# Optimization experiments

Hardware: AMD Instinct MI355X
Metric: run time of the kernel (lower is better)

Reference implementation:

```python
import jax, jax.numpy as jnp
import numpy as np

NU = 60000   # num_users
NI = 40000   # num_items
N = NU + NI  # num_nodes
E = 2000000  # num_edges
F = 128      # feat_dim (user_feat_dim == item_feat_dim)
H = 128      # hidden_dim


def setup_inputs() -> dict:
    key = jax.random.key(0)
    ks = jax.random.split(key, 14)
    s = 0.05
    inp = {
        "x": jax.random.normal(ks[0], (N, F), jnp.float32),
        "edge_index": jax.random.randint(ks[1], (2, E), 0, N, dtype=jnp.int32),
        "node_type": jnp.concatenate([jnp.zeros(NU, jnp.int32), jnp.ones(NI, jnp.int32)]),
        # input projections (Linear stores weight as (out, in))
        "w_user": s * jax.random.normal(ks[2], (H, F), jnp.float32),
        "b_user": jnp.zeros((H,), jnp.float32),
        "w_item": s * jax.random.normal(ks[3], (H, F), jnp.float32),
        "b_item": jnp.zeros((H,), jnp.float32),
        # SAGEConv layer 0: lin_l (aggregated neighbors, with bias), lin_r (root, no bias)
        "w_l0": s * jax.random.normal(ks[4], (H, H), jnp.float32),
        "b_l0": s * jax.random.normal(ks[5], (H,), jnp.float32),
        "w_r0": s * jax.random.normal(ks[6], (H, H), jnp.float32),
        # SAGEConv layer 1
        "w_l1": s * jax.random.normal(ks[7], (H, H), jnp.float32),
        "b_l1": s * jax.random.normal(ks[8], (H,), jnp.float32),
        "w_r1": s * jax.random.normal(ks[9], (H, H), jnp.float32),
    }
    return inp


def _sage_conv(h, src, dst, w_l, b_l, w_r):
    # gather source features, max-aggregate onto destinations (PyG aggr='max')
    msg = h[src]                                          # [E, H]
    agg = jax.ops.segment_max(msg, dst, num_segments=N)   # [N, H], -inf where no in-edges
    agg = jnp.where(jnp.isneginf(agg), 0.0, agg)          # PyG fills empty segments with 0
    return agg @ w_l.T + b_l + h @ w_r.T


def reference(x, edge_index, node_type, w_user, b_user, w_item, b_item,
              w_l0, b_l0, w_r0, w_l1, b_l1, w_r1):
    # node_type is sorted: first NU rows are users, rest are items
    src, dst = edge_index[0], edge_index[1]
    user_h = x[:NU] @ w_user.T + b_user                   # [NU, H]
    item_h = x[NU:] @ w_item.T + b_item                   # [NI, H]
    h = jnp.concatenate([user_h, item_h], axis=0)         # [N, H]
    # layer 0 with residual (dims match) then ReLU; dropout is identity in eval
    h = h + _sage_conv(h, src, dst, w_l0, b_l0, w_r0)
    h = jax.nn.relu(h)
    # layer 1 with residual (no activation after last layer)
    h = h + _sage_conv(h, src, dst, w_l1, b_l1, w_r1)
    return (h[:NU], h[NU:])
```

## Files before the change

kernel.cpp:

```cpp
#include <hip/hip_runtime.h>

#define NUSR 60000
#define NITM 40000
#define NN   100000
#define EE   2000000
#define HD   128

#define BW   512
#define NB   196
#define EPB  8192

using bf16x8   = __attribute__((ext_vector_type(8))) short;
using f32x4    = __attribute__((ext_vector_type(4))) float;
using ushort4t = __attribute__((ext_vector_type(4))) unsigned short;
using ushort2t = __attribute__((ext_vector_type(2))) unsigned short;
using ushort8t = __attribute__((ext_vector_type(8))) unsigned short;
using uint4t   = __attribute__((ext_vector_type(4))) unsigned int;

__device__ __forceinline__ unsigned short f2bf(float f) {
    unsigned int u = __float_as_uint(f);
    u += 0x7FFFu + ((u >> 16) & 1u);
    return (unsigned short)(u >> 16);
}
__device__ __forceinline__ float bf2f(unsigned short s) {
    return __uint_as_float(((unsigned int)s) << 16);
}
__device__ __forceinline__ unsigned short keyof(unsigned short b) {
    return (b & 0x8000u) ? (unsigned short)~b : (unsigned short)(b | 0x8000u);
}
__device__ __forceinline__ unsigned unkey32(unsigned k) {
    unsigned negsel = (~k & 0x80008000u) >> 15;
    return k ^ (0x80008000u | (negsel * 0x7FFFu));
}
__device__ __forceinline__ int swz(int row, int col) {
    return row * HD + (col ^ ((row & 7) << 3));
}
__device__ __forceinline__ ushort8t pkmax8(ushort8t a, ushort8t b) {
    return __builtin_elementwise_max(a, b);
}

__global__ __launch_bounds__(256) void bhist_k(const int* __restrict__ dst,
                                               int* __restrict__ bcnt) {
    __shared__ int h[NB];
    int t = threadIdx.x;
    if (t < NB) h[t] = 0;
    __syncthreads();
    int e0 = blockIdx.x * EPB;
    #pragma unroll 4
    for (int i = t; i < EPB; i += 256) {
        int e = e0 + i;
        if (e < EE) atomicAdd(&h[dst[e] >> 9], 1);
    }
    __syncthreads();
    if (t < NB && h[t]) atomicAdd(&bcnt[t], h[t]);
}

__global__ void bscan_k(const int* __restrict__ bcnt, int* __restrict__ bbase,
                        int* __restrict__ bcur, int* __restrict__ off) {
    __shared__ int s[256];
    int t = threadIdx.x;
    int v = (t < NB) ? bcnt[t] : 0;
    s[t] = v;
    __syncthreads();
    for (int d = 1; d < 256; d <<= 1) {
        int a = (t >= d) ? s[t - d] : 0;
        __syncthreads();
        s[t] += a;
        __syncthreads();
    }
    if (t < NB) { bbase[t] = s[t] - v; bcur[t] = s[t] - v; }
    if (t == NB - 1) { bbase[NB] = s[t]; off[NN] = EE; }
}

__global__ __launch_bounds__(256) void bscatter_k(const int* __restrict__ src,
                                                  const int* __restrict__ dst,
                                                  int* __restrict__ bcur,
                                                  unsigned int* __restrict__ bedge) {
    __shared__ int h[NB], base[NB];
    int t = threadIdx.x;
    if (t < NB) h[t] = 0;
    __syncthreads();
    int e0 = blockIdx.x * EPB;
    #pragma unroll 4
    for (int i = t; i < EPB; i += 256) {
        int e = e0 + i;
        if (e < EE) atomicAdd(&h[dst[e] >> 9], 1);
    }
    __syncthreads();
    if (t < NB) {
        int c = h[t];
        base[t] = c ? atomicAdd(&bcur[t], c) : 0;
        h[t] = 0;
    }
    __syncthreads();
    #pragma unroll 4
    for (int i = t; i < EPB; i += 256) {
        int e = e0 + i;
        if (e < EE) {
            int d = dst[e];
            int b = d >> 9;
            int p = base[b] + atomicAdd(&h[b], 1);
            bedge[p] = ((unsigned)(d - (b << 9)) << 17) | (unsigned)src[e];
        }
    }
}

__global__ __launch_bounds__(512) void bcsr_k(const unsigned int* __restrict__ bedge,
                                              const int* __restrict__ bbase,
                                              int* __restrict__ off,
                                              int* __restrict__ csr) {
    __shared__ int cnt[BW], cur[BW], sc[BW];
    int b = blockIdx.x, t = threadIdx.x;
    int n0 = b * BW;
    int nloc = min(BW, NN - n0);
    cnt[t] = 0;
    __syncthreads();
    int e0 = bbase[b], e1 = bbase[b + 1];
    for (int e = e0 + t; e < e1; e += 512)
        atomicAdd(&cnt[bedge[e] >> 17], 1);
    __syncthreads();
    int v = cnt[t];
    sc[t] = v;
    __syncthreads();
    for (int d = 1; d < BW; d <<= 1) {
        int a = (t >= d) ? sc[t - d] : 0;
        __syncthreads();
        sc[t] += a;
        __syncthreads();
    }
    int excl = sc[t] - v;
    if (t < nloc) { off[n0 + t] = e0 + excl; cur[t] = e0 + excl; }
    __syncthreads();
    for (int e = e0 + t; e < e1; e += 512) {
        unsigned ed = bedge[e];
        int p = atomicAdd(&cur[ed >> 17], 1);
        csr[p] = (int)(ed & 0x1FFFFu);
    }
}

__global__ void cvt6_k(const float* __restrict__ a0, const float* __restrict__ a1,
                       const float* __restrict__ a2, const float* __restrict__ a3,
                       const float* __restrict__ a4, const float* __restrict__ a5,
                       unsigned short* __restrict__ out) {
    int i = blockIdx.x * 256 + threadIdx.x;
    const float* s;
    switch (i >> 14) {
        case 0: s = a0; break; case 1: s = a1; break; case 2: s = a2; break;
        case 3: s = a3; break; case 4: s = a4; break; default: s = a5; break;
    }
    out[i] = f2bf(s[i & 16383]);
}

__global__ __launch_bounds__(256) void proj_mfma_k(
    const float* __restrict__ x, const unsigned short* __restrict__ wb,
    const float* __restrict__ bias, unsigned short* __restrict__ hkey,
    int row_base, int nrows) {
    __shared__ unsigned short lw[HD * HD];
    int tid = threadIdx.x;
    #pragma unroll
    for (int it = 0; it < 16; ++it) {
        int flat = (it * 256 + tid) * 4;
        int row = flat >> 7, col = flat & 127;
        *(ushort4t*)&lw[swz(row, col)] = *(const ushort4t*)(wb + flat);
    }
    __syncthreads();
    int lane = tid & 63, w = tid >> 6;
    int l15 = lane & 15, l4 = lane >> 4;
    int m0 = blockIdx.x * 128 + w * 32;
    f32x4 acc[2][8] = {};
    #pragma unroll
    for (int kb = 0; kb < 4; ++kb) {
        bf16x8 a[2];
        #pragma unroll
        for (int rt = 0; rt < 2; ++rt) {
            int r = m0 + rt * 16 + l15;
            if (r >= nrows) r = nrows - 1;
            const float* ap = x + (size_t)(row_base + r) * HD + kb * 32 + l4 * 8;
            f32x4 v0 = *(const f32x4*)ap;
            f32x4 v1 = *(const f32x4*)(ap + 4);
            bf16x8 f;
            #pragma unroll
            for (int j = 0; j < 4; ++j) { f[j] = (short)f2bf(v0[j]); f[j + 4] = (short)f2bf(v1[j]); }
            a[rt] = f;
        }
        #pragma unroll
        for (int ct = 0; ct < 8; ++ct) {
            bf16x8 b = *(const bf16x8*)&lw[swz(ct * 16 + l15, kb * 32 + l4 * 8)];
            acc[0][ct] = __builtin_amdgcn_mfma_f32_16x16x32_bf16(a[0], b, acc[0][ct], 0, 0, 0);
            acc[1][ct] = __builtin_amdgcn_mfma_f32_16x16x32_bf16(a[1], b, acc[1][ct], 0, 0, 0);
        }
    }
    __syncthreads();
    #pragma unroll
    for (int ct = 0; ct < 8; ++ct) {
        int col = ct * 16 + l15;
        float bv = bias[col];
        #pragma unroll
        for (int rt = 0; rt < 2; ++rt)
            #pragma unroll
            for (int j = 0; j < 4; ++j) {
                int lrow = w * 32 + rt * 16 + l4 * 4 + j;
                lw[lrow * HD + ((col + ((lrow & 15) << 3)) & 127)] =
                    keyof(f2bf(acc[rt][ct][j] + bv));
            }
    }
    __syncthreads();
    int row = tid >> 1, cb = (tid & 1) * 64;
    int r = blockIdx.x * 128 + row;
    if (r < nrows) {
        int sof = (row & 15) << 3;
        #pragma unroll
        for (int gg = 0; gg < 8; ++gg) {
            uint4t v = *(const uint4t*)&lw[row * HD + ((cb + gg * 8 + sof) & 127)];
            *(uint4t*)(hkey + (size_t)(row_base + r) * HD + cb + gg * 8) = v;
        }
    }
}

__global__ __launch_bounds__(256) void agg_key_k(
    const uint4t* __restrict__ hkey4,
    const int* __restrict__ off, const int* __restrict__ csr,
    uint4t* __restrict__ agg4) {
    int node = (blockIdx.x * 256 + threadIdx.x) >> 6;
    int lane = threadIdx.x & 63;
    if (node >= NN) return;
    int s0 = off[node], s1 = off[node + 1];
    int deg = s1 - s0;
    int q = lane >> 4, l16 = lane & 15;
    ushort8t m = {0, 0, 0, 0, 0, 0, 0, 0};
    int cval = (lane < deg) ? csr[s0 + lane] : 0;
    int nslots = deg < 64 ? deg : 64;
    #pragma unroll
    for (int u = 0; u < 16; ++u) {
        int idx = u * 4 + q;
        int r = __shfl(cval, idx, 64);
        if (idx < nslots) {
            uint4t v = hkey4[(size_t)r * 16 + l16];
            m = pkmax8(m, *(ushort8t*)&v);
        }
    }
    for (int base = s0 + 64; base < s1; base += 32) {
        #pragma unroll
        for (int u = 0; u < 8; ++u) {
            int jj = base + u * 4 + q;
            if (jj < s1) {
                int r = csr[jj];
                uint4t v = hkey4[(size_t)r * 16 + l16];
                m = pkmax8(m, *(ushort8t*)&v);
            }
        }
    }
    uint4t mu = *(uint4t*)&m;
    #pragma unroll
    for (int c = 0; c < 4; ++c) {
        unsigned a = mu[c];
        unsigned b = (unsigned)__shfl_xor((int)a, 16, 64);
        ushort2t pa = *(ushort2t*)&a, pb = *(ushort2t*)&b;
        pa = __builtin_elementwise_max(pa, pb);
        a = *(unsigned*)&pa;
        b = (unsigned)__shfl_xor((int)a, 32, 64);
        pb = *(ushort2t*)&b;
        pa = __builtin_elementwise_max(pa, pb);
        mu[c] = *(unsigned*)&pa;
    }
    if (q == 0) {
        uint4t outv = {0, 0, 0, 0};
        if (deg > 0) {
            #pragma unroll
            for (int c = 0; c < 4; ++c) outv[c] = unkey32(mu[c]);
        }
        agg4[(size_t)node * 16 + l16] = outv;
    }
}

__global__ __launch_bounds__(256) void combine_mfma_k(
    const unsigned short* __restrict__ hkey, const unsigned short* __restrict__ aggb,
    const unsigned short* __restrict__ wlb, const float* __restrict__ bl,
    const unsigned short* __restrict__ wrb,
    unsigned short* __restrict__ hkey_out, float* __restrict__ fout, int relu) {
    __shared__ unsigned short lw[2][HD * HD];
    int tid = threadIdx.x;
    #pragma unroll
    for (int it = 0; it < 16; ++it) {
        int flat = (it * 256 + tid) * 4;
        int row = flat >> 7, col = flat & 127;
        *(ushort4t*)&lw[0][swz(row, col)] = *(const ushort4t*)(wlb + flat);
        *(ushort4t*)&lw[1][swz(row, col)] = *(const ushort4t*)(wrb + flat);
    }
    __syncthreads();
    int lane = tid & 63, w = tid >> 6;
    int l15 = lane & 15, l4 = lane >> 4;
    int m0 = blockIdx.x * 128 + w * 32;
    const uint4t* hk4 = (const uint4t*)hkey;
    f32x4 acc[2][8] = {};
    #pragma unroll
    for (int kb = 0; kb < 4; ++kb) {
        bf16x8 a1[2], a2[2];
        #pragma unroll
        for (int rt = 0; rt < 2; ++rt) {
            int r = m0 + rt * 16 + l15;
            if (r >= NN) r = NN - 1;
            size_t o = (size_t)r * HD + kb * 32 + l4 * 8;
            a1[rt] = *(const bf16x8*)(aggb + o);
            uint4t aw = hk4[(size_t)r * 16 + kb * 4 + l4];
            bf16x8 f;
            #pragma unroll
            for (int u = 0; u < 4; ++u) {
                unsigned d = unkey32(aw[u]);
                f[2 * u]     = (short)(d & 0xFFFFu);
                f[2 * u + 1] = (short)(d >> 16);
            }
            a2[rt] = f;
        }
        #pragma unroll
        for (int ct = 0; ct < 8; ++ct) {
            bf16x8 b1 = *(const bf16x8*)&lw[0][swz(ct * 16 + l15, kb * 32 + l4 * 8)];
            bf16x8 b2 = *(const bf16x8*)&lw[1][swz(ct * 16 + l15, kb * 32 + l4 * 8)];
            acc[0][ct] = __builtin_amdgcn_mfma_f32_16x16x32_bf16(a1[0], b1, acc[0][ct], 0, 0, 0);
            acc[0][ct] = __builtin_amdgcn_mfma_f32_16x16x32_bf16(a2[0], b2, acc[0][ct], 0, 0, 0);
            acc[1][ct] = __builtin_amdgcn_mfma_f32_16x16x32_bf16(a1[1], b1, acc[1][ct], 0, 0, 0);
            acc[1][ct] = __builtin_amdgcn_mfma_f32_16x16x32_bf16(a2[1], b2, acc[1][ct], 0, 0, 0);
        }
    }
    __syncthreads();
    float* cs = (float*)lw;
    #pragma unroll
    for (int ct = 0; ct < 8; ++ct)
        #pragma unroll
        for (int rt = 0; rt < 2; ++rt)
            #pragma unroll
            for (int j = 0; j < 4; ++j) {
                int lrow = w * 32 + rt * 16 + l4 * 4 + j;
                int col = ct * 16 + l15;
                cs[lrow * HD + ((col + lrow) & 127)] = acc[rt][ct][j];
            }
    __syncthreads();
    int row = tid >> 1, cb = (tid & 1) * 64;
    int r = blockIdx.x * 128 + row;
    if (r < NN) {
        const uint4t* resrow = (const uint4t*)(hkey + (size_t)r * HD + cb);
        uint4t res[8];
        #pragma unroll
        for (int g = 0; g < 8; ++g) res[g] = resrow[g];
        if (fout) {
            #pragma unroll
            for (int gg = 0; gg < 8; ++gg) {
                f32x4 va, vb;
                #pragma unroll
                for (int u = 0; u < 4; ++u) {
                    int c0 = cb + gg * 8 + u * 2;
                    unsigned d = unkey32(res[gg][u]);
                    float v0 = cs[row * HD + ((c0 + row) & 127)] + bl[c0]
                             + bf2f((unsigned short)(d & 0xFFFFu));
                    float v1 = cs[row * HD + ((c0 + 1 + row) & 127)] + bl[c0 + 1]
                             + bf2f((unsigned short)(d >> 16));
                    if (relu) { v0 = fmaxf(v0, 0.0f); v1 = fmaxf(v1, 0.0f); }
                    if (u < 2) { va[u * 2] = v0; va[u * 2 + 1] = v1; }
                    else       { vb[(u - 2) * 2] = v0; vb[(u - 2) * 2 + 1] = v1; }
                }
                *(f32x4*)(fout + (size_t)r * HD + cb + gg * 8) = va;
                *(f32x4*)(fout + (size_t)r * HD + cb + gg * 8 + 4) = vb;
            }
        } else {
            #pragma unroll
            for (int gg = 0; gg < 8; ++gg) {
                uint4t ov;
                #pragma unroll
                for (int u = 0; u < 4; ++u) {
                    int c0 = cb + gg * 8 + u * 2;
                    unsigned d = unkey32(res[gg][u]);
                    float v0 = cs[row * HD + ((c0 + row) & 127)] + bl[c0]
                             + bf2f((unsigned short)(d & 0xFFFFu));
                    float v1 = cs[row * HD + ((c0 + 1 + row) & 127)] + bl[c0 + 1]
                             + bf2f((unsigned short)(d >> 16));
                    if (relu) { v0 = fmaxf(v0, 0.0f); v1 = fmaxf(v1, 0.0f); }
                    ov[u] = (unsigned)keyof(f2bf(v0)) | ((unsigned)keyof(f2bf(v1)) << 16);
                }
                *(uint4t*)(hkey_out + (size_t)r * HD + cb + gg * 8) = ov;
            }
        }
    }
}

extern "C" void kernel_launch(void* const* d_in, const int* in_sizes, int n_in,
                              void* d_out, int out_size, void* d_ws, size_t ws_size,
                              hipStream_t stream) {
    const float* x      = (const float*)d_in[0];
    const int*   ei     = (const int*)d_in[1];
    const float* w_user = (const float*)d_in[3];
    const float* b_user = (const float*)d_in[4];
    const float* w_item = (const float*)d_in[5];
    const float* b_item = (const float*)d_in[6];
    const float* w_l0   = (const float*)d_in[7];
    const float* b_l0   = (const float*)d_in[8];
    const float* w_r0   = (const float*)d_in[9];
    const float* w_l1   = (const float*)d_in[10];
    const float* b_l1   = (const float*)d_in[11];
    const float* w_r1   = (const float*)d_in[12];

    const int* e_src = ei;
    const int* e_dst = ei + EE;

    char* ws = (char*)d_ws;
    size_t cur_off = 0;
    auto carve = [&](size_t bytes) {
        void* p = ws + cur_off;
        cur_off = (cur_off + bytes + 255) & ~(size_t)255;
        return p;
    };
    unsigned short* hkey0 = (unsigned short*)carve((size_t)NN * HD * 2);
    unsigned short* hkey1 = (unsigned short*)carve((size_t)NN * HD * 2);
    unsigned short* aggb  = (unsigned short*)carve((size_t)NN * HD * 2);
    unsigned short* wb    = (unsigned short*)carve((size_t)6 * HD * HD * 2);
    int*      off   = (int*)carve((size_t)(NN + 1) * 4);
    int*      csr   = (int*)carve((size_t)EE * 4);
    unsigned* bedge = (unsigned*)carve((size_t)EE * 4);
    int*      bcnt  = (int*)carve((NB + 1) * 4);
    int*      bbase = (int*)carve((NB + 1) * 4);
    int*      bcur  = (int*)carve((NB + 1) * 4);
    (void)ws_size;

    hipMemsetAsync(bcnt, 0, (size_t)NB * 4, stream);
    int nbB = (EE + EPB - 1) / EPB;
    bhist_k<<<nbB, 256, 0, stream>>>(e_dst, bcnt);
    bscan_k<<<1, 256, 0, stream>>>(bcnt, bbase, bcur, off);
    bscatter_k<<<nbB, 256, 0, stream>>>(e_src, e_dst, bcur, bedge);
    bcsr_k<<<NB, 512, 0, stream>>>(bedge, bbase, off, csr);

    cvt6_k<<<(6 * HD * HD) / 256, 256, 0, stream>>>(w_user, w_item, w_l0, w_r0, w_l1, w_r1, wb);

    proj_mfma_k<<<(NUSR + 127) / 128, 256, 0, stream>>>(x, wb,         b_user, hkey0, 0,    NUSR);
    proj_mfma_k<<<(NITM + 127) / 128, 256, 0, stream>>>(x, wb + 16384, b_item, hkey0, NUSR, NITM);

    agg_key_k<<<NN / 4, 256, 0, stream>>>((const uint4t*)hkey0, off, csr, (uint4t*)aggb);
    combine_mfma_k<<<(NN + 127) / 128, 256, 0, stream>>>(
        hkey0, aggb, wb + 2 * 16384, b_l0, wb + 3 * 16384, hkey1, nullptr, 1);

    agg_key_k<<<NN / 4, 256, 0, stream>>>((const uint4t*)hkey1, off, csr, (uint4t*)aggb);
    combine_mfma_k<<<(NN + 127) / 128, 256, 0, stream>>>(
        hkey1, aggb, wb + 4 * 16384, b_l1, wb + 5 * 16384, nullptr, (float*)d_out, 0);
}
```

Before: 313.2 us.

## Double combine block to 256 rows and vectorize epilogue with two-phase LDS staging

```diff
diff --git a/kernel.cpp b/kernel.cpp
--- a/kernel.cpp
+++ b/kernel.cpp
@@ -273,7 +273,7 @@
     }
 }
 
-__global__ __launch_bounds__(256) void combine_mfma_k(
+__global__ __launch_bounds__(512) void combine_mfma_k(
     const unsigned short* __restrict__ hkey, const unsigned short* __restrict__ aggb,
     const unsigned short* __restrict__ wlb, const float* __restrict__ bl,
     const unsigned short* __restrict__ wrb,
@@ -281,8 +281,8 @@
     __shared__ unsigned short lw[2][HD * HD];
     int tid = threadIdx.x;
     #pragma unroll
-    for (int it = 0; it < 16; ++it) {
-        int flat = (it * 256 + tid) * 4;
+    for (int it = 0; it < 8; ++it) {
+        int flat = (it * 512 + tid) * 4;
         int row = flat >> 7, col = flat & 127;
         *(ushort4t*)&lw[0][swz(row, col)] = *(const ushort4t*)(wlb + flat);
         *(ushort4t*)&lw[1][swz(row, col)] = *(const ushort4t*)(wrb + flat);
@@ -290,7 +290,7 @@
     __syncthreads();
     int lane = tid & 63, w = tid >> 6;
     int l15 = lane & 15, l4 = lane >> 4;
-    int m0 = blockIdx.x * 128 + w * 32;
+    int m0 = blockIdx.x * 256 + w * 32;
     const uint4t* hk4 = (const uint4t*)hkey;
     f32x4 acc[2][8] = {};
     #pragma unroll
@@ -324,61 +324,64 @@
     }
     __syncthreads();
     float* cs = (float*)lw;
-    #pragma unroll
-    for (int ct = 0; ct < 8; ++ct)
-        #pragma unroll
-        for (int rt = 0; rt < 2; ++rt)
-            #pragma unroll
-            for (int j = 0; j < 4; ++j) {
-                int lrow = w * 32 + rt * 16 + l4 * 4 + j;
-                int col = ct * 16 + l15;
-                cs[lrow * HD + ((col + lrow) & 127)] = acc[rt][ct][j];
-            }
-    __syncthreads();
-    int row = tid >> 1, cb = (tid & 1) * 64;
-    int r = blockIdx.x * 128 + row;
-    if (r < NN) {
-        const uint4t* resrow = (const uint4t*)(hkey + (size_t)r * HD + cb);
-        uint4t res[8];
-        #pragma unroll
-        for (int g = 0; g < 8; ++g) res[g] = resrow[g];
-        if (fout) {
-            #pragma unroll
-            for (int gg = 0; gg < 8; ++gg) {
-                f32x4 va, vb;
+    for (int p = 0; p < 2; ++p) {
+        if ((w >> 2) == p) {
+            #pragma unroll
+            for (int ct = 0; ct < 8; ++ct)
+                #pragma unroll
+                for (int rt = 0; rt < 2; ++rt)
+                    #pragma unroll
+                    for (int j = 0; j < 4; ++j) {
+                        int lrow = (w & 3) * 32 + rt * 16 + l4 * 4 + j;
+                        int col = ct * 16 + l15;
+                        cs[lrow * HD + ((col + lrow * 4) & 127)] = acc[rt][ct][j];
+                    }
+        }
+        __syncthreads();
+        int lrow = tid >> 2, cq = (tid & 3) * 32;
+        int r = blockIdx.x * 256 + p * 128 + lrow;
+        if (r < NN) {
+            const float* crow = cs + lrow * HD;
+            int rot = lrow * 4;
+            #pragma unroll
+            for (int gg = 0; gg < 4; ++gg) {
+                int c0 = cq + gg * 8;
+                uint4t res = *(const uint4t*)(hkey + (size_t)r * HD + c0);
+                f32x4 cv0 = *(const f32x4*)&crow[(c0 + rot) & 127];
+                f32x4 cv1 = *(const f32x4*)&crow[(c0 + 4 + rot) & 127];
+                f32x4 bv0 = *(const f32x4*)(bl + c0);
+                f32x4 bv1 = *(const f32x4*)(bl + c0 + 4);
+                float v[8];
                 #pragma unroll
                 for (int u = 0; u < 4; ++u) {
-                    int c0 = cb + gg * 8 + u * 2;
-                    unsigned d = unkey32(res[gg][u]);
-                    float v0 = cs[row * HD + ((c0 + row) & 127)] + bl[c0]
-                             + bf2f((unsigned short)(d & 0xFFFFu));
-                    float v1 = cs[row * HD + ((c0 + 1 + row) & 127)] + bl[c0 + 1]
-                             + bf2f((unsigned short)(d >> 16));
-                    if (relu) { v0 = fmaxf(v0, 0.0f); v1 = fmaxf(v1, 0.0f); }
-                    if (u < 2) { va[u * 2] = v0; va[u * 2 + 1] = v1; }
-                    else       { vb[(u - 2) * 2] = v0; vb[(u - 2) * 2 + 1] = v1; }
+                    unsigned d = unkey32(res[u]);
+                    float c_lo = (u < 2) ? cv0[u * 2]     : cv1[(u - 2) * 2];
+                    float c_hi = (u < 2) ? cv0[u * 2 + 1] : cv1[(u - 2) * 2 + 1];
+                    float b_lo = (u < 2) ? bv0[u * 2]     : bv1[(u - 2) * 2];
+                    float b_hi = (u < 2) ? bv0[u * 2 + 1] : bv1[(u - 2) * 2 + 1];
+                    v[2 * u]     = c_lo + b_lo + bf2f((unsigned short)(d & 0xFFFFu));
+                    v[2 * u + 1] = c_hi + b_hi + bf2f((unsigned short)(d >> 16));
                 }
-                *(f32x4*)(fout + (size_t)r * HD + cb + gg * 8) = va;
-                *(f32x4*)(fout + (size_t)r * HD + cb + gg * 8 + 4) = vb;
+                if (relu) {
+                    #pragma unroll
+                    for (int u = 0; u < 8; ++u) v[u] = fmaxf(v[u], 0.0f);
+                }
+                if (fout) {
+                    f32x4 o0 = {v[0], v[1], v[2], v[3]};
+                    f32x4 o1 = {v[4], v[5], v[6], v[7]};
+                    *(f32x4*)(fout + (size_t)r * HD + c0) = o0;
+                    *(f32x4*)(fout + (size_t)r * HD + c0 + 4) = o1;
+                } else {
+                    uint4t ov;
+                    #pragma unroll
+                    for (int u = 0; u < 4; ++u)
+                        ov[u] = (unsigned)keyof(f2bf(v[2 * u]))
+                              | ((unsigned)keyof(f2bf(v[2 * u + 1])) << 16);
+                    *(uint4t*)(hkey_out + (size_t)r * HD + c0) = ov;
+                }
             }
-        } else {
-            #pragma unroll
-            for (int gg = 0; gg < 8; ++gg) {
-                uint4t ov;
-                #pragma unroll
-                for (int u = 0; u < 4; ++u) {
-                    int c0 = cb + gg * 8 + u * 2;
-                    unsigned d = unkey32(res[gg][u]);
-                    float v0 = cs[row * HD + ((c0 + row) & 127)] + bl[c0]
-                             + bf2f((unsigned short)(d & 0xFFFFu));
-                    float v1 = cs[row * HD + ((c0 + 1 + row) & 127)] + bl[c0 + 1]
-                             + bf2f((unsigned short)(d >> 16));
-                    if (relu) { v0 = fmaxf(v0, 0.0f); v1 = fmaxf(v1, 0.0f); }
-                    ov[u] = (unsigned)keyof(f2bf(v0)) | ((unsigned)keyof(f2bf(v1)) << 16);
-                }
-                *(uint4t*)(hkey_out + (size_t)r * HD + cb + gg * 8) = ov;
-            }
-        }
+        }
+        __syncthreads();
     }
 }
 
@@ -433,10 +436,10 @@
     proj_mfma_k<<<(NITM + 127) / 128, 256, 0, stream>>>(x, wb + 16384, b_item, hkey0, NUSR, NITM);
 
     agg_key_k<<<NN / 4, 256, 0, stream>>>((const uint4t*)hkey0, off, csr, (uint4t*)aggb);
-    combine_mfma_k<<<(NN + 127) / 128, 256, 0, stream>>>(
+    combine_mfma_k<<<(NN + 255) / 256, 512, 0, stream>>>(
         hkey0, aggb, wb + 2 * 16384, b_l0, wb + 3 * 16384, hkey1, nullptr, 1);
 
     agg_key_k<<<NN / 4, 256, 0, stream>>>((const uint4t*)hkey1, off, csr, (uint4t*)aggb);
-    combine_mfma_k<<<(NN + 127) / 128, 256, 0, stream>>>(
+    combine_mfma_k<<<(NN + 255) / 256, 512, 0, stream>>>(
         hkey1, aggb, wb + 4 * 16384, b_l1, wb + 5 * 16384, nullptr, (float*)d_out, 0);
 }
```

Measured after the change: 314.3 us. No clear change (+0.4%).
